# Optimization experiments

Hardware: AMD Instinct MI355X
Metric: run time of the kernel (lower is better)

Reference implementation:

```python
import jax, jax.numpy as jnp
import numpy as np

H = 8      # n_heads
HD = 64    # per-head channels (out_channels in __init__, before *= n_heads)


def setup_inputs() -> dict:
    key = jax.random.key(0)
    ks = jax.random.split(key, 10)
    B, C, N = 4, 256, 2048
    O = H * HD
    s = 1.0 / np.sqrt(C).astype(np.float32)
    return {
        "x": jax.random.normal(ks[0], (B, C, N), dtype=jnp.float32),
        "y": jax.random.normal(ks[1], (B, C, N), dtype=jnp.float32),
        "Wq": jax.random.normal(ks[2], (O, C), dtype=jnp.float32) * s,
        "bq": jnp.zeros((O,), dtype=jnp.float32),
        "Wk": jax.random.normal(ks[3], (O, C), dtype=jnp.float32) * s,
        "bk": jnp.zeros((O,), dtype=jnp.float32),
        "Wv": jax.random.normal(ks[4], (O, C), dtype=jnp.float32) * s,
        "bv": jnp.zeros((O,), dtype=jnp.float32),
        "Wp": jax.random.normal(ks[5], (HD, C), dtype=jnp.float32) * s,  # residual projection, bias=False
        "gamma": jax.random.uniform(ks[6], (H, 1, 1, 1), dtype=jnp.float32) + 0.001,
    }


def _conv1x1(W, b, t):
    # 1x1 Conv1d: (O,C) x (B,C,N) -> (B,O,N)
    out = jnp.einsum('oc,bcn->bon', W, t)
    return out if b is None else out + b[None, :, None]


def _heads(t):
    # (B, H*HD, N) -> (H, B, N, HD); channel split into contiguous per-head chunks
    B, _, N = t.shape
    return t.reshape(B, H, HD, N).transpose(1, 0, 3, 2)


def reference(x, y, Wq, bq, Wk, bk, Wv, bv, Wp, gamma):
    # q/k/v projections via 1x1 convs (kernel_size=1, 'stride_effective' padding => same length)
    q = _heads(_conv1x1(Wq, bq, x))   # (H,B,N,HD)
    k = _heads(_conv1x1(Wk, bk, y))   # (H,B,N,HD)
    v = _heads(_conv1x1(Wv, bv, y))   # (H,B,N,HD)

    # energy = bmm(Q, K^T); softmax over last dim (no mask)
    energy = jnp.einsum('hbnd,hbmd->hbnm', q, k)          # (H,B,N,N)
    attn = jax.nn.softmax(energy, axis=-1)

    # out = bmm(attention.transpose(-2,-1), V)  (note the transpose in the original)
    out = jnp.einsum('hbnm,hbnd->hbmd', attn, v)          # (H,B,N,HD)

    # gamma-weighted residual blend with projected y
    yp = _conv1x1(Wp, None, y).transpose(0, 2, 1)         # (B,N,HD)
    g = gamma.reshape(H, 1, 1, 1)
    out = (g * out + yp[None]) / (1.0 + g)                # (H,B,N,HD)
    return out
```

## Files before the change

kernel.cpp:

```cpp
#include <hip/hip_runtime.h>
#include <math.h>
#include <stdint.h>

#define B_DIM 4
#define C_DIM 256
#define N_DIM 2048
#define H_DIM 8
#define HD    64
#define HB    32
#define NTOK  (B_DIM * N_DIM)
#define LOG2E 1.44269504f

typedef __attribute__((ext_vector_type(8))) short bf16x8;
typedef __attribute__((ext_vector_type(4))) float f32x4;

static __device__ __forceinline__ short f2bf(float f) {
    unsigned u = __builtin_bit_cast(unsigned, f);
    u += 0x7fffu + ((u >> 16) & 1u);
    return (short)(u >> 16);
}
static __device__ __forceinline__ float bf2f(short s) {
    unsigned u = ((unsigned)(unsigned short)s) << 16;
    return __builtin_bit_cast(float, u);
}
static __device__ __forceinline__ float fx2(float x) {
#if __has_builtin(__builtin_amdgcn_exp2f)
    return __builtin_amdgcn_exp2f(x);
#else
    return exp2f(x);
#endif
}
static __device__ __forceinline__ unsigned pk_bf16(float a, float b) {
#if __has_builtin(__builtin_amdgcn_cvt_pk_bf16_f32)
    auto v = __builtin_amdgcn_cvt_pk_bf16_f32(a, b);
    return __builtin_bit_cast(unsigned, v);
#else
    unsigned ua = __builtin_bit_cast(unsigned, a);
    unsigned ub = __builtin_bit_cast(unsigned, b);
    return ((ua + 0x8000u) >> 16) | ((ub + 0x8000u) & 0xffff0000u);
#endif
}

static __device__ __forceinline__ void gll16(const void* g, void* ldsbase, int lane) {
#if __has_builtin(__builtin_amdgcn_global_load_lds)
    __builtin_amdgcn_global_load_lds(
        (const __attribute__((address_space(1))) void*)(uintptr_t)(g),
        (__attribute__((address_space(3))) void*)(uintptr_t)(ldsbase), 16, 0, 0);
#else
    *(bf16x8*)((char*)ldsbase + lane * 16) = *(const bf16x8*)g;
#endif
}

#define MFMA16(A, Bv, Cv) __builtin_amdgcn_mfma_f32_16x16x32_bf16(A, Bv, Cv, 0, 0, 0)


__global__ __launch_bounds__(256) void cast_all(
    const float* __restrict__ X, const float* __restrict__ Y,
    const float* __restrict__ Wq, const float* __restrict__ Wk,
    const float* __restrict__ Wv, const float* __restrict__ Wp,
    short* __restrict__ XS, short* __restrict__ YS,
    short* __restrict__ WSx, short* __restrict__ WSy)
{
    const int z = blockIdx.z;
    const int t = threadIdx.x;

    if (z == 8) {
        int base = (blockIdx.y * 32 + blockIdx.x) * 256 + t;
#pragma unroll
        for (int rep = 0; rep < 2; ++rep) {
            int gid = base + rep * 32768;
            if (gid >= 51200) break;
            int lane = gid & 63, chunk = gid >> 6;
            int lo = lane & 15, quad = lane >> 4;
            const float* src; short* dst;
            if (chunk < 256) {
                int ot = chunk >> 3, ks = chunk & 7;
                src = Wq + (size_t)(ot * 16 + lo) * C_DIM + ks * 32 + quad * 8;
                dst = WSx + (size_t)chunk * 512 + lane * 8;
            } else {
                int ch = chunk - 256;
                int ot = ch >> 3, ks = ch & 7;
                int row = ot * 16 + lo;
                const float* basep = (row < 512) ? (Wk + (size_t)row * C_DIM)
                                   : (row < 1024) ? (Wv + (size_t)(row - 512) * C_DIM)
                                                  : (Wp + (size_t)(row - 1024) * C_DIM);
                src = basep + ks * 32 + quad * 8;
                dst = WSy + (size_t)ch * 512 + lane * 8;
            }
            bf16x8 o;
#pragma unroll
            for (int j = 0; j < 8; ++j) o[j] = f2bf(src[j]);
            *(bf16x8*)dst = o;
        }
        return;
    }

    const float* src = (z < 4) ? X : Y;
    short* dst = (z < 4) ? XS : YS;
    const int b = z & 3, c0 = blockIdx.y * 64, n0 = blockIdx.x * 64;
    __shared__ float L[64][65];
    for (int i = t; i < 4096; i += 256) {
        int cc = i >> 6, nn = i & 63;
        L[cc][nn] = src[((size_t)b * C_DIM + c0 + cc) * N_DIM + n0 + nn];
    }
    __syncthreads();
#pragma unroll
    for (int half = 0; half < 2; ++half) {
        int cid = half * 256 + t;
        int lane = cid & 63, fi = cid >> 6;
        int ksl = fi & 1, rtl = fi >> 1;
        int lo = lane & 15, quad = lane >> 4;
        bf16x8 o;
#pragma unroll
        for (int j = 0; j < 8; ++j) o[j] = f2bf(L[ksl * 32 + quad * 8 + j][rtl * 16 + lo]);
        int rt = b * 128 + (n0 >> 4) + rtl;
        int ks = (c0 >> 5) + ksl;
        *(bf16x8*)(dst + ((size_t)(rt * 8 + ks) * 64 + lane) * 8) = o;
    }
}

__global__ __launch_bounds__(256) void proj_all(
    const short* __restrict__ WSx, const short* __restrict__ WSy,
    const short* __restrict__ XS, const short* __restrict__ YS,
    const float* __restrict__ bq, const float* __restrict__ bk,
    const float* __restrict__ bv,
    short* __restrict__ QS, short* __restrict__ KS,
    short* __restrict__ VSu, float* __restrict__ Yo)
{
    const int oy = blockIdx.y;
    const bool isq = oy < 8;
    const short* WS = isq ? WSx : WSy;
    const short* Xs = isq ? XS : YS;
    const int oyl = isq ? oy : oy - 8;
    const int o0 = oyl * 64;
    const int tok0 = blockIdx.x * 128;
    const int t = threadIdx.x, wave = t >> 6, lane = t & 63;
    const int lo = lane & 15, quad = lane >> 4;

    __shared__ __align__(16) char smem[34816];

    const int ot = oyl * 4 + wave;
    const int rt0 = tok0 >> 4;
    const f32x4 czero = {0.f, 0.f, 0.f, 0.f};

    f32x4 acc[8];
#pragma unroll
    for (int i = 0; i < 8; ++i) acc[i] = czero;

#pragma unroll 2
    for (int ks = 0; ks < 8; ++ks) {
        bf16x8 a = *(const bf16x8*)(WS + ((size_t)(ot * 8 + ks) * 64 + lane) * 8);
#pragma unroll
        for (int nt = 0; nt < 8; ++nt) {
            bf16x8 bx = *(const bf16x8*)(Xs + ((size_t)((rt0 + nt) * 8 + ks) * 64 + lane) * 8);
            acc[nt] = MFMA16(a, bx, acc[nt]);
        }
    }

    const int b = tok0 >> 11;
    const int n0b = tok0 & (N_DIM - 1);

    if (oy < 16) {
        short* T = (short*)smem;
        const float* bias = isq ? bq : bk;
        const float scale = isq ? LOG2E : 1.f;
        float bvr[4];
#pragma unroll
        for (int r = 0; r < 4; ++r) bvr[r] = bias[o0 + wave * 16 + quad * 4 + r];
#pragma unroll
        for (int nt = 0; nt < 8; ++nt) {
            short4 pk;
            pk.x = f2bf((acc[nt][0] + bvr[0]) * scale);
            pk.y = f2bf((acc[nt][1] + bvr[1]) * scale);
            pk.z = f2bf((acc[nt][2] + bvr[2]) * scale);
            pk.w = f2bf((acc[nt][3] + bvr[3]) * scale);
            *(short4*)(T + (nt * 16 + lo) * 72 + wave * 16 + quad * 4) = pk;
        }
        __syncthreads();
        const int h = oyl;
        const int hb = h * 4 + b;
        short* dst = isq ? QS : KS;
#pragma unroll
        for (int s = 0; s < 4; ++s) {
            int cid = s * 256 + t;
            int ln = cid & 63, fi = cid >> 6;
            int ksd = fi & 1, rtl = fi >> 1;
            bf16x8 v = *(const bf16x8*)(T + (rtl * 16 + (ln & 15)) * 72 + ksd * 32 + (ln >> 4) * 8);
            *(bf16x8*)(dst + (((size_t)(hb * 128 + (n0b >> 4) + rtl) * 2 + ksd) * 512 + ln * 8)) = v;
        }
    } else if (oy < 24) {
        short* T2 = (short*)smem;
        float bvr[4];
#pragma unroll
        for (int r = 0; r < 4; ++r) bvr[r] = bv[o0 - 512 + wave * 16 + quad * 4 + r];
#pragma unroll
        for (int nt = 0; nt < 8; ++nt)
#pragma unroll
            for (int r = 0; r < 4; ++r) {
                int ol = wave * 16 + quad * 4 + r;
                T2[ol * 136 + nt * 16 + lo] = f2bf(acc[nt][r] + bvr[r]);
            }
        __syncthreads();
        const int h = oy - 16;
        const int hb = h * 4 + b;
#pragma unroll
        for (int s = 0; s < 4; ++s) {
            int cid = s * 256 + t;
            int ln = cid & 63, fi = cid >> 6;
            int dt = fi & 3, ksd = (fi >> 2) & 1, nbl = fi >> 3;
            int dl = dt * 16 + (ln & 15);
            int tkl = nbl * 64 + ksd * 32 + (ln >> 4) * 8;
            bf16x8 v = *(const bf16x8*)(T2 + dl * 136 + tkl);
            int nbg = (n0b >> 6) + nbl;
            *(bf16x8*)(VSu + ((size_t)(((hb * 32 + nbg) * 2 + ksd) * 4 + dt) * 64 + ln) * 8) = v;
        }
    } else {
        float* T3 = (float*)smem;
#pragma unroll
        for (int nt = 0; nt < 8; ++nt) {
            float4 f;
            f.x = acc[nt][0]; f.y = acc[nt][1]; f.z = acc[nt][2]; f.w = acc[nt][3];
            *(float4*)(T3 + (nt * 16 + lo) * 68 + wave * 16 + quad * 4) = f;
        }
        __syncthreads();
#pragma unroll
        for (int s = 0; s < 8; ++s) {
            int cid = s * 256 + t;
            int row = cid >> 4, c4 = (cid & 15) * 4;
            float4 f = *(const float4*)(T3 + row * 68 + c4);
            *(float4*)(Yo + ((size_t)(tok0 + row)) * 64 + c4) = f;
        }
    }
}

__global__ __launch_bounds__(256, 4) void rowsum_mfma(
    const short* __restrict__ QS, const short* __restrict__ KS,
    float* __restrict__ RSp, float* __restrict__ RSpW)
{
    const int id = blockIdx.x;
    const int hb = ((id & 7) << 2) | ((id >> 3) & 3);
    const int zq = (id >> 5) & 3;
    const int n0 = (id >> 7) * 256;
    const int t = threadIdx.x, wave = t >> 6, lane = t & 63;
    const int lo = lane & 15, quad = lane >> 4;
    const f32x4 czero = {0.f, 0.f, 0.f, 0.f};

    bf16x8 a0[4], a1[4];
#pragma unroll
    for (int s = 0; s < 4; ++s) {
        int rt = (n0 >> 4) + s * 4 + wave;
        a0[s] = *(const bf16x8*)(QS + ((size_t)(hb * 128 + rt) * 2 + 0) * 512 + lane * 8);
        a1[s] = *(const bf16x8*)(QS + ((size_t)(hb * 128 + rt) * 2 + 1) * 512 + lane * 8);
    }

    float sm[4][4];
#pragma unroll
    for (int s = 0; s < 4; ++s)
#pragma unroll
        for (int r = 0; r < 4; ++r) sm[s][r] = 0.f;

    const short* kp = KS + ((size_t)(hb * 128) * 2) * 512 + lane * 8
                    + (size_t)zq * (N_DIM / 4 / 16) * 2 * 512;
    for (int m0 = 0; m0 < N_DIM / 4; m0 += 64) {
#pragma unroll
        for (int mt = 0; mt < 4; ++mt) {
            bf16x8 b0 = *(const bf16x8*)(kp + (mt * 2 + 0) * 512);
            bf16x8 b1 = *(const bf16x8*)(kp + (mt * 2 + 1) * 512);
#pragma unroll
            for (int s = 0; s < 4; ++s) {
                f32x4 c = MFMA16(a0[s], b0, czero);
                c = MFMA16(a1[s], b1, c);
#pragma unroll
                for (int r = 0; r < 4; ++r) sm[s][r] += fx2(c[r]);
            }
        }
        kp += 8 * 512;
    }

#pragma unroll
    for (int sft = 1; sft < 16; sft <<= 1)
#pragma unroll
        for (int s = 0; s < 4; ++s)
#pragma unroll
            for (int r = 0; r < 4; ++r) sm[s][r] += __shfl_xor(sm[s][r], sft);

    if (lo == 0) {
        float* dst = (zq < 2) ? (RSp  + (size_t)zq * HB * N_DIM)
                              : (RSpW + (size_t)(zq - 2) * HB * N_DIM);
#pragma unroll
        for (int s = 0; s < 4; ++s) {
            int row = n0 + s * 64 + wave * 16 + quad * 4;
#pragma unroll
            for (int r = 0; r < 4; ++r)
                dst[(size_t)hb * N_DIM + row + r] = sm[s][r];
        }
    }
}

__global__ __launch_bounds__(256) void v_scale(
    const short* __restrict__ VSu, const float* __restrict__ RSp,
    const float* __restrict__ RSpW, short* __restrict__ VS)
{
    int t = blockIdx.x * 256 + threadIdx.x;
    int lane = t & 63, fidx = t >> 6;
    int ks = (fidx >> 2) & 1, nb = (fidx >> 3) & 31, hb = fidx >> 8;
    int n = nb * 64 + ks * 32 + (lane >> 4) * 8;
    bf16x8 v = *(const bf16x8*)(VSu + (size_t)t * 8);
    const float* r0 = RSp  + (size_t)hb * N_DIM + n;
    const float* r1 = r0 + (size_t)HB * N_DIM;
    const float* r2 = RSpW + (size_t)hb * N_DIM + n;
    const float* r3 = r2 + (size_t)HB * N_DIM;
    bf16x8 o;
#pragma unroll
    for (int j = 0; j < 8; ++j)
        o[j] = f2bf(bf2f(v[j]) / ((r0[j] + r1[j]) + (r2[j] + r3[j])));
    *(bf16x8*)(VS + (size_t)t * 8) = o;
}

__global__ __launch_bounds__(512, 4) void attnout_mfma(
    const short* __restrict__ QS, const short* __restrict__ KS,
    const short* __restrict__ VS,
    short* __restrict__ PA0, short* __restrict__ PA1)
{
    const int id = blockIdx.x;
    const int hb = ((id & 7) << 2) | ((id >> 3) & 3);
    const int z = (id >> 5) & 1;
    const int m0 = (id >> 6) * 128;

    __shared__ __align__(16) char smem[49152];
    short* Pl = (short*)smem;
    char* Qst = smem + 16384;
    char* Vst = smem + 32768;

    const int t = threadIdx.x, wave = t >> 6, lane = t & 63;
    const int lo = lane & 15, quad = lane >> 4;
    const f32x4 czero = {0.f, 0.f, 0.f, 0.f};

    bf16x8 bk0, bk1;
    {
        int rt = (m0 >> 4) + wave;
        bk0 = *(const bf16x8*)(KS + ((size_t)(hb * 128 + rt) * 2 + 0) * 512 + lane * 8);
        bk1 = *(const bf16x8*)(KS + ((size_t)(hb * 128 + rt) * 2 + 1) * 512 + lane * 8);
    }

    f32x4 oacc[4];
#pragma unroll
    for (int dt = 0; dt < 4; ++dt) oacc[dt] = czero;

    const short* qsrc = QS + ((size_t)(hb * 128 + z * 64) * 2) * 512 + lane * 8;
    const short* vsrc = VS + ((size_t)(hb * 32 + z * 16) * 8) * 512 + lane * 8;
    short* prow = Pl + (wave * 16 + lo) * 64;
    const int lh = lo & 7;
    const int NIT = N_DIM / 2 / 64;

    f32x4 c[4];

    gll16(qsrc + (size_t)wave * 512,       Qst + wave * 1024, lane);
    gll16(qsrc + (size_t)(8 + wave) * 512, Qst + 8192 + wave * 1024, lane);
    gll16(vsrc + (size_t)wave * 512,       Vst + wave * 1024, lane);
    __syncthreads();
#pragma unroll
    for (int nt = 0; nt < 4; ++nt) {
        bf16x8 a0 = *(const bf16x8*)(Qst + (nt * 2 + 0) * 1024 + lane * 16);
        bf16x8 a1 = *(const bf16x8*)(Qst + (nt * 2 + 1) * 1024 + lane * 16);
        c[nt] = MFMA16(a0, bk0, czero);
        c[nt] = MFMA16(a1, bk1, c[nt]);
    }
    __syncthreads();

    for (int i = 0; i < NIT - 1; ++i) {
        gll16(qsrc + ((size_t)(i + 2) * 8 + wave) * 512,
              Qst + (i & 1) * 8192 + wave * 1024, lane);
        gll16(vsrc + ((size_t)(i + 1) * 8 + wave) * 512,
              Vst + ((i + 1) & 1) * 8192 + wave * 1024, lane);
#pragma unroll
        for (int nt = 0; nt < 4; ++nt) {
            uint2 pk;
            pk.x = pk_bf16(fx2(c[nt][0]), fx2(c[nt][1]));
            pk.y = pk_bf16(fx2(c[nt][2]), fx2(c[nt][3]));
            int chunk = nt * 2 + (quad >> 1);
            *(uint2*)(prow + (((chunk ^ lh) << 3) | ((quad & 1) << 2))) = pk;
        }
        {
            const char* Qb = Qst + ((i + 1) & 1) * 8192;
            __builtin_amdgcn_s_setprio(1);
#pragma unroll
            for (int nt = 0; nt < 4; ++nt) {
                bf16x8 a0 = *(const bf16x8*)(Qb + (nt * 2 + 0) * 1024 + lane * 16);
                bf16x8 a1 = *(const bf16x8*)(Qb + (nt * 2 + 1) * 1024 + lane * 16);
                c[nt] = MFMA16(a0, bk0, czero);
                c[nt] = MFMA16(a1, bk1, c[nt]);
            }
            __builtin_amdgcn_s_setprio(0);
        }
        {
            const char* vb = Vst + (i & 1) * 8192;
#pragma unroll
            for (int ks = 0; ks < 2; ++ks) {
                bf16x8 ap = *(const bf16x8*)(prow + (((ks * 4 + quad) ^ lh) << 3));
#pragma unroll
                for (int dt = 0; dt < 4; ++dt) {
                    bf16x8 bv = *(const bf16x8*)(vb + (ks * 4 + dt) * 1024 + lane * 16);
                    oacc[dt] = MFMA16(ap, bv, oacc[dt]);
                }
            }
        }
        __syncthreads();
    }

#pragma unroll
    for (int nt = 0; nt < 4; ++nt) {
        uint2 pk;
        pk.x = pk_bf16(fx2(c[nt][0]), fx2(c[nt][1]));
        pk.y = pk_bf16(fx2(c[nt][2]), fx2(c[nt][3]));
        int chunk = nt * 2 + (quad >> 1);
        *(uint2*)(prow + (((chunk ^ lh) << 3) | ((quad & 1) << 2))) = pk;
    }
    {
        const char* vb = Vst + ((NIT - 1) & 1) * 8192;
#pragma unroll
        for (int ks = 0; ks < 2; ++ks) {
            bf16x8 ap = *(const bf16x8*)(prow + (((ks * 4 + quad) ^ lh) << 3));
#pragma unroll
            for (int dt = 0; dt < 4; ++dt) {
                bf16x8 bv = *(const bf16x8*)(vb + (ks * 4 + dt) * 1024 + lane * 16);
                oacc[dt] = MFMA16(ap, bv, oacc[dt]);
            }
        }
    }

    short* PA = z ? PA1 : PA0;
    float* T = (float*)smem;
    __syncthreads();
#pragma unroll
    for (int dt = 0; dt < 4; ++dt)
#pragma unroll
        for (int r = 0; r < 4; ++r)
            T[(wave * 16 + quad * 4 + r) * 68 + dt * 16 + lo] = oacc[dt][r];
    __syncthreads();
#pragma unroll
    for (int it = 0; it < 2; ++it) {
        int idx = it * 512 + t;
        int rowl = idx >> 3, dg = (idx & 7) * 8;
        float4 f0 = *(const float4*)(T + rowl * 68 + dg);
        float4 f1 = *(const float4*)(T + rowl * 68 + dg + 4);
        uint4 o;
        o.x = pk_bf16(f0.x, f0.y);
        o.y = pk_bf16(f0.z, f0.w);
        o.z = pk_bf16(f1.x, f1.y);
        o.w = pk_bf16(f1.z, f1.w);
        int m = m0 + rowl;
        *(uint4*)(PA + ((size_t)(hb * N_DIM + m)) * 64 + dg) = o;
    }
}

__global__ __launch_bounds__(256) void combine_out(
    const short* __restrict__ PA0, const short* __restrict__ PA1,
    const float* __restrict__ YP, const float* __restrict__ gamma,
    float* __restrict__ out)
{
    size_t flat = ((size_t)blockIdx.x * 256 + threadIdx.x) * 8;
    int d  = (int)(flat & 63);
    int n  = (int)((flat >> 6) & (N_DIM - 1));
    int hb = (int)(flat >> 17);
    int h = hb >> 2, b = hb & 3;
    float g = gamma[h];
    float inv = 1.f / (1.f + g);
    float gi = g * inv;
    bf16x8 p0 = *(const bf16x8*)(PA0 + flat);
    bf16x8 p1 = *(const bf16x8*)(PA1 + flat);
    const float* yp = YP + ((size_t)b * N_DIM + n) * HD + d;
    float o[8];
#pragma unroll
    for (int j = 0; j < 8; ++j)
        o[j] = gi * (bf2f(p0[j]) + bf2f(p1[j])) + inv * yp[j];
    float4 o0 = {o[0], o[1], o[2], o[3]};
    float4 o1 = {o[4], o[5], o[6], o[7]};
    *(float4*)(out + flat) = o0;
    *(float4*)(out + flat + 4) = o1;
}

extern "C" void kernel_launch(void* const* d_in, const int* in_sizes, int n_in,
                              void* d_out, int out_size, void* d_ws, size_t ws_size,
                              hipStream_t stream) {
    const float* x     = (const float*)d_in[0];
    const float* y     = (const float*)d_in[1];
    const float* Wq    = (const float*)d_in[2];
    const float* bq    = (const float*)d_in[3];
    const float* Wk    = (const float*)d_in[4];
    const float* bk    = (const float*)d_in[5];
    const float* Wv    = (const float*)d_in[6];
    const float* bv    = (const float*)d_in[7];
    const float* Wp    = (const float*)d_in[8];
    const float* gamma = (const float*)d_in[9];
    float* out = (float*)d_out;

    const size_t XEL  = (size_t)B_DIM * C_DIM * N_DIM;
    const size_t QKV  = (size_t)HB * N_DIM * HD;

    short* XS  = (short*)d_ws;
    short* YS  = XS + XEL;
    short* WSx = YS + XEL;
    short* WSy = WSx + 512 * C_DIM;
    short* QS  = WSy + 1088 * C_DIM;
    short* KS  = QS + QKV;
    short* VSu = KS + QKV;
    short* VS  = VSu + QKV;
    float* YPb = (float*)(VS + QKV);
    float* RSp = YPb + (size_t)B_DIM * N_DIM * HD;
    short* PA0 = XS;
    short* PA1 = VSu;
    float* RSpW = (float*)WSx;

    dim3 blk(256);
    cast_all<<<dim3(N_DIM / 64, C_DIM / 64, 9), blk, 0, stream>>>(
        x, y, Wq, Wk, Wv, Wp, XS, YS, WSx, WSy);

    proj_all<<<dim3(NTOK / 128, 25), blk, 0, stream>>>(
        WSx, WSy, XS, YS, bq, bk, bv, QS, KS, VSu, YPb);

    rowsum_mfma<<<dim3(1024), blk, 0, stream>>>(QS, KS, RSp, RSpW);
    v_scale<<<dim3(2048), blk, 0, stream>>>(VSu, RSp, RSpW, VS);
    attnout_mfma<<<dim3(1024), dim3(512), 0, stream>>>(QS, KS, VS, PA0, PA1);
    combine_out<<<dim3(2048), blk, 0, stream>>>(PA0, PA1, YPb, gamma, out);
}
```

Measured before the change: 188.9 us.

## Switch attention kernels to 32x32x16 MFMA with register-resident P via permlane swap

Moves the rowsum and attention-output kernels from 16x16x32 MFMA tiles to 32x32x16 tiles, and changes the Q/K/V fragment layouts written by the projection kernel to match. In attnout, the exp'd score tile is now converted directly into the A-operand of the PV MFMA in registers using permlane32 swaps, instead of being staged through LDS. That removes the P-tile LDS round trip and lowers the instruction count per FLOP. Blocks shrink from 512 to 256 threads with each wave covering 32 rows, which raises register pressure and may reduce occupancy.

```diff
diff --git a/kernel.cpp b/kernel.cpp
--- a/kernel.cpp
+++ b/kernel.cpp
@@ -13,6 +13,8 @@
 
 typedef __attribute__((ext_vector_type(8))) short bf16x8;
 typedef __attribute__((ext_vector_type(4))) float f32x4;
+typedef __attribute__((ext_vector_type(16))) float f32x16;
+typedef __attribute__((ext_vector_type(4))) unsigned u32x4;
 
 static __device__ __forceinline__ short f2bf(float f) {
     unsigned u = __builtin_bit_cast(unsigned, f);
@@ -40,6 +42,19 @@
     return ((ua + 0x8000u) >> 16) | ((ub + 0x8000u) & 0xffff0000u);
 #endif
 }
+static __device__ __forceinline__ void pl32swap(unsigned &a, unsigned &b) {
+#if __has_builtin(__builtin_amdgcn_permlane32_swap)
+    typedef __attribute__((ext_vector_type(2))) int i32x2_t;
+    i32x2_t r = __builtin_amdgcn_permlane32_swap((int)a, (int)b, false, false);
+    a = (unsigned)r[0]; b = (unsigned)r[1];
+#else
+    unsigned sa = __shfl_xor(a, 32), sb = __shfl_xor(b, 32);
+    bool hi = (threadIdx.x & 32) != 0;
+    unsigned na = hi ? sb : a;
+    unsigned nb = hi ? b : sa;
+    a = na; b = nb;
+#endif
+}
 
 static __device__ __forceinline__ void gll16(const void* g, void* ldsbase, int lane) {
 #if __has_builtin(__builtin_amdgcn_global_load_lds)
@@ -52,6 +67,7 @@
 }
 
 #define MFMA16(A, Bv, Cv) __builtin_amdgcn_mfma_f32_16x16x32_bf16(A, Bv, Cv, 0, 0, 0)
+#define MFMA32(A, Bv, Cv) __builtin_amdgcn_mfma_f32_32x32x16_bf16(A, Bv, Cv, 0, 0, 0)
 
 
 __global__ __launch_bounds__(256) void cast_all(
@@ -184,9 +200,11 @@
         for (int s = 0; s < 4; ++s) {
             int cid = s * 256 + t;
             int ln = cid & 63, fi = cid >> 6;
-            int ksd = fi & 1, rtl = fi >> 1;
-            bf16x8 v = *(const bf16x8*)(T + (rtl * 16 + (ln & 15)) * 72 + ksd * 32 + (ln >> 4) * 8);
-            *(bf16x8*)(dst + (((size_t)(hb * 128 + (n0b >> 4) + rtl) * 2 + ksd) * 512 + ln * 8)) = v;
+            int ks = fi & 3, nt2l = fi >> 2;
+            bf16x8 v = *(const bf16x8*)(T + (nt2l * 32 + (ln & 31)) * 72
+                                          + ks * 16 + ((ln >> 5) << 3));
+            size_t frag = ((size_t)(hb * 64) + (n0b >> 5) + nt2l) * 4 + ks;
+            *(bf16x8*)(dst + frag * 512 + ln * 8) = v;
         }
     } else if (oy < 24) {
         short* T2 = (short*)smem;
@@ -207,12 +225,11 @@
         for (int s = 0; s < 4; ++s) {
             int cid = s * 256 + t;
             int ln = cid & 63, fi = cid >> 6;
-            int dt = fi & 3, ksd = (fi >> 2) & 1, nbl = fi >> 3;
-            int dl = dt * 16 + (ln & 15);
-            int tkl = nbl * 64 + ksd * 32 + (ln >> 4) * 8;
-            bf16x8 v = *(const bf16x8*)(T2 + dl * 136 + tkl);
-            int nbg = (n0b >> 6) + nbl;
-            *(bf16x8*)(VSu + ((size_t)(((hb * 32 + nbg) * 2 + ksd) * 4 + dt) * 64 + ln) * 8) = v;
+            int dt2 = fi & 1, nk = (fi >> 1) & 3, nbl = fi >> 3;
+            bf16x8 v = *(const bf16x8*)(T2 + (dt2 * 32 + (ln & 31)) * 136
+                                           + nbl * 64 + nk * 16 + ((ln >> 5) << 3));
+            size_t frag = (((size_t)(hb * 32) + (n0b >> 6) + nbl) * 4 + nk) * 2 + dt2;
+            *(bf16x8*)(VSu + frag * 512 + ln * 8) = v;
         }
     } else {
         float* T3 = (float*)smem;
@@ -242,58 +259,60 @@
     const int zq = (id >> 5) & 3;
     const int n0 = (id >> 7) * 256;
     const int t = threadIdx.x, wave = t >> 6, lane = t & 63;
-    const int lo = lane & 15, quad = lane >> 4;
-    const f32x4 czero = {0.f, 0.f, 0.f, 0.f};
-
-    bf16x8 a0[4], a1[4];
-#pragma unroll
-    for (int s = 0; s < 4; ++s) {
-        int rt = (n0 >> 4) + s * 4 + wave;
-        a0[s] = *(const bf16x8*)(QS + ((size_t)(hb * 128 + rt) * 2 + 0) * 512 + lane * 8);
-        a1[s] = *(const bf16x8*)(QS + ((size_t)(hb * 128 + rt) * 2 + 1) * 512 + lane * 8);
-    }
-
-    float sm[4][4];
-#pragma unroll
-    for (int s = 0; s < 4; ++s)
-#pragma unroll
-        for (int r = 0; r < 4; ++r) sm[s][r] = 0.f;
-
-    const short* kp = KS + ((size_t)(hb * 128) * 2) * 512 + lane * 8
-                    + (size_t)zq * (N_DIM / 4 / 16) * 2 * 512;
-    for (int m0 = 0; m0 < N_DIM / 4; m0 += 64) {
-#pragma unroll
-        for (int mt = 0; mt < 4; ++mt) {
-            bf16x8 b0 = *(const bf16x8*)(kp + (mt * 2 + 0) * 512);
-            bf16x8 b1 = *(const bf16x8*)(kp + (mt * 2 + 1) * 512);
-#pragma unroll
-            for (int s = 0; s < 4; ++s) {
-                f32x4 c = MFMA16(a0[s], b0, czero);
-                c = MFMA16(a1[s], b1, c);
-#pragma unroll
-                for (int r = 0; r < 4; ++r) sm[s][r] += fx2(c[r]);
-            }
-        }
-        kp += 8 * 512;
-    }
-
-#pragma unroll
-    for (int sft = 1; sft < 16; sft <<= 1)
-#pragma unroll
-        for (int s = 0; s < 4; ++s)
-#pragma unroll
-            for (int r = 0; r < 4; ++r) sm[s][r] += __shfl_xor(sm[s][r], sft);
-
-    if (lo == 0) {
+    const int hi = lane >> 5;
+    f32x16 czero16;
+#pragma unroll
+    for (int r = 0; r < 16; ++r) czero16[r] = 0.f;
+
+    bf16x8 qf[2][4];
+    const short* qb = QS + ((size_t)(hb * 64 + (n0 >> 5) + wave * 2)) * 4 * 512 + lane * 8;
+#pragma unroll
+    for (int tt = 0; tt < 2; ++tt)
+#pragma unroll
+        for (int ks = 0; ks < 4; ++ks)
+            qf[tt][ks] = *(const bf16x8*)(qb + (tt * 4 + ks) * 512);
+
+    float sm[2][16];
+#pragma unroll
+    for (int tt = 0; tt < 2; ++tt)
+#pragma unroll
+        for (int r = 0; r < 16; ++r) sm[tt][r] = 0.f;
+
+    const short* kp = KS + ((size_t)(hb * 64 + zq * 16)) * 4 * 512 + lane * 8;
+    for (int mt = 0; mt < 16; ++mt) {
+        bf16x8 kf[4];
+#pragma unroll
+        for (int ks = 0; ks < 4; ++ks)
+            kf[ks] = *(const bf16x8*)(kp + (mt * 4 + ks) * 512);
+#pragma unroll
+        for (int tt = 0; tt < 2; ++tt) {
+            f32x16 cc = czero16;
+#pragma unroll
+            for (int ks = 0; ks < 4; ++ks) cc = MFMA32(qf[tt][ks], kf[ks], cc);
+#pragma unroll
+            for (int r = 0; r < 16; ++r) sm[tt][r] += fx2(cc[r]);
+        }
+    }
+
+#pragma unroll
+    for (int sft = 1; sft < 32; sft <<= 1)
+#pragma unroll
+        for (int tt = 0; tt < 2; ++tt)
+#pragma unroll
+            for (int r = 0; r < 16; ++r) sm[tt][r] += __shfl_xor(sm[tt][r], sft);
+
+    if ((lane & 31) == 0) {
         float* dst = (zq < 2) ? (RSp  + (size_t)zq * HB * N_DIM)
                               : (RSpW + (size_t)(zq - 2) * HB * N_DIM);
 #pragma unroll
-        for (int s = 0; s < 4; ++s) {
-            int row = n0 + s * 64 + wave * 16 + quad * 4;
-#pragma unroll
-            for (int r = 0; r < 4; ++r)
-                dst[(size_t)hb * N_DIM + row + r] = sm[s][r];
-        }
+        for (int tt = 0; tt < 2; ++tt)
+#pragma unroll
+            for (int g = 0; g < 4; ++g) {
+                int n = n0 + wave * 64 + tt * 32 + g * 8 + hi * 4;
+                float4 v = {sm[tt][g * 4 + 0], sm[tt][g * 4 + 1],
+                            sm[tt][g * 4 + 2], sm[tt][g * 4 + 3]};
+                *(float4*)(dst + (size_t)hb * N_DIM + n) = v;
+            }
     }
 }
 
@@ -303,8 +322,9 @@
 {
     int t = blockIdx.x * 256 + threadIdx.x;
     int lane = t & 63, fidx = t >> 6;
-    int ks = (fidx >> 2) & 1, nb = (fidx >> 3) & 31, hb = fidx >> 8;
-    int n = nb * 64 + ks * 32 + (lane >> 4) * 8;
+    int dt2 = fidx & 1; (void)dt2;
+    int nk = (fidx >> 1) & 3, nb = (fidx >> 3) & 31, hb = fidx >> 8;
+    int n = nb * 64 + nk * 16 + ((lane >> 5) << 3);
     bf16x8 v = *(const bf16x8*)(VSu + (size_t)t * 8);
     const float* r0 = RSp  + (size_t)hb * N_DIM + n;
     const float* r1 = r0 + (size_t)HB * N_DIM;
@@ -317,7 +337,7 @@
     *(bf16x8*)(VS + (size_t)t * 8) = o;
 }
 
-__global__ __launch_bounds__(512, 4) void attnout_mfma(
+__global__ __launch_bounds__(256, 3) void attnout_mfma(
     const short* __restrict__ QS, const short* __restrict__ KS,
     const short* __restrict__ VS,
     short* __restrict__ PA0, short* __restrict__ PA1)
@@ -327,120 +347,145 @@
     const int z = (id >> 5) & 1;
     const int m0 = (id >> 6) * 128;
 
-    __shared__ __align__(16) char smem[49152];
-    short* Pl = (short*)smem;
-    char* Qst = smem + 16384;
-    char* Vst = smem + 32768;
+    __shared__ __align__(16) char smem[34816];
+    char* Qst = smem;
+    char* Vst = smem + 16384;
 
     const int t = threadIdx.x, wave = t >> 6, lane = t & 63;
-    const int lo = lane & 15, quad = lane >> 4;
-    const f32x4 czero = {0.f, 0.f, 0.f, 0.f};
-
-    bf16x8 bk0, bk1;
+    const f32x4 cz4 = {0.f, 0.f, 0.f, 0.f}; (void)cz4;
+    f32x16 czero16;
+#pragma unroll
+    for (int r = 0; r < 16; ++r) czero16[r] = 0.f;
+
+    bf16x8 kf[4];
     {
-        int rt = (m0 >> 4) + wave;
-        bk0 = *(const bf16x8*)(KS + ((size_t)(hb * 128 + rt) * 2 + 0) * 512 + lane * 8);
-        bk1 = *(const bf16x8*)(KS + ((size_t)(hb * 128 + rt) * 2 + 1) * 512 + lane * 8);
-    }
-
-    f32x4 oacc[4];
-#pragma unroll
-    for (int dt = 0; dt < 4; ++dt) oacc[dt] = czero;
-
-    const short* qsrc = QS + ((size_t)(hb * 128 + z * 64) * 2) * 512 + lane * 8;
-    const short* vsrc = VS + ((size_t)(hb * 32 + z * 16) * 8) * 512 + lane * 8;
-    short* prow = Pl + (wave * 16 + lo) * 64;
-    const int lh = lo & 7;
+        const short* kbase = KS + ((size_t)(hb * 64 + (m0 >> 5) + wave)) * 4 * 512 + lane * 8;
+#pragma unroll
+        for (int ks = 0; ks < 4; ++ks)
+            kf[ks] = *(const bf16x8*)(kbase + ks * 512);
+    }
+
+    f32x16 oacc[2];
+#pragma unroll
+    for (int dt2 = 0; dt2 < 2; ++dt2) oacc[dt2] = czero16;
+
+    const short* qsrc = QS + ((size_t)(hb * 64 + z * 32)) * 4 * 512 + lane * 8;
+    const short* vsrc = VS + ((size_t)(hb * 32 + z * 16)) * 8 * 512 + lane * 8;
     const int NIT = N_DIM / 2 / 64;
 
-    f32x4 c[4];
-
-    gll16(qsrc + (size_t)wave * 512,       Qst + wave * 1024, lane);
-    gll16(qsrc + (size_t)(8 + wave) * 512, Qst + 8192 + wave * 1024, lane);
-    gll16(vsrc + (size_t)wave * 512,       Vst + wave * 1024, lane);
+    f32x16 c[2];
+    bf16x8 pa[4];
+
+    gll16(qsrc + (size_t)wave * 512,            Qst + wave * 1024, lane);
+    gll16(qsrc + (size_t)(wave + 4) * 512,      Qst + (wave + 4) * 1024, lane);
+    gll16(qsrc + (size_t)(8 + wave) * 512,      Qst + 8192 + wave * 1024, lane);
+    gll16(qsrc + (size_t)(8 + wave + 4) * 512,  Qst + 8192 + (wave + 4) * 1024, lane);
+    gll16(vsrc + (size_t)wave * 512,            Vst + wave * 1024, lane);
+    gll16(vsrc + (size_t)(wave + 4) * 512,      Vst + (wave + 4) * 1024, lane);
     __syncthreads();
 #pragma unroll
-    for (int nt = 0; nt < 4; ++nt) {
-        bf16x8 a0 = *(const bf16x8*)(Qst + (nt * 2 + 0) * 1024 + lane * 16);
-        bf16x8 a1 = *(const bf16x8*)(Qst + (nt * 2 + 1) * 1024 + lane * 16);
-        c[nt] = MFMA16(a0, bk0, czero);
-        c[nt] = MFMA16(a1, bk1, c[nt]);
+    for (int tt = 0; tt < 2; ++tt) {
+        f32x16 cc = czero16;
+#pragma unroll
+        for (int ks = 0; ks < 4; ++ks) {
+            bf16x8 a = *(const bf16x8*)(Qst + (tt * 4 + ks) * 1024 + lane * 16);
+            cc = MFMA32(a, kf[ks], cc);
+        }
+        c[tt] = cc;
     }
     __syncthreads();
 
     for (int i = 0; i < NIT - 1; ++i) {
         gll16(qsrc + ((size_t)(i + 2) * 8 + wave) * 512,
               Qst + (i & 1) * 8192 + wave * 1024, lane);
+        gll16(qsrc + ((size_t)(i + 2) * 8 + wave + 4) * 512,
+              Qst + (i & 1) * 8192 + (wave + 4) * 1024, lane);
         gll16(vsrc + ((size_t)(i + 1) * 8 + wave) * 512,
               Vst + ((i + 1) & 1) * 8192 + wave * 1024, lane);
-#pragma unroll
-        for (int nt = 0; nt < 4; ++nt) {
-            uint2 pk;
-            pk.x = pk_bf16(fx2(c[nt][0]), fx2(c[nt][1]));
-            pk.y = pk_bf16(fx2(c[nt][2]), fx2(c[nt][3]));
-            int chunk = nt * 2 + (quad >> 1);
-            *(uint2*)(prow + (((chunk ^ lh) << 3) | ((quad & 1) << 2))) = pk;
+        gll16(vsrc + ((size_t)(i + 1) * 8 + wave + 4) * 512,
+              Vst + ((i + 1) & 1) * 8192 + (wave + 4) * 1024, lane);
+#pragma unroll
+        for (int tt = 0; tt < 2; ++tt) {
+#pragma unroll
+            for (int half = 0; half < 2; ++half) {
+                unsigned w01 = pk_bf16(fx2(c[tt][half * 8 + 0]), fx2(c[tt][half * 8 + 1]));
+                unsigned w23 = pk_bf16(fx2(c[tt][half * 8 + 2]), fx2(c[tt][half * 8 + 3]));
+                unsigned w45 = pk_bf16(fx2(c[tt][half * 8 + 4]), fx2(c[tt][half * 8 + 5]));
+                unsigned w67 = pk_bf16(fx2(c[tt][half * 8 + 6]), fx2(c[tt][half * 8 + 7]));
+                pl32swap(w01, w45);
+                pl32swap(w23, w67);
+                u32x4 f = {w01, w23, w45, w67};
+                pa[tt * 2 + half] = __builtin_bit_cast(bf16x8, f);
+            }
         }
         {
             const char* Qb = Qst + ((i + 1) & 1) * 8192;
             __builtin_amdgcn_s_setprio(1);
 #pragma unroll
-            for (int nt = 0; nt < 4; ++nt) {
-                bf16x8 a0 = *(const bf16x8*)(Qb + (nt * 2 + 0) * 1024 + lane * 16);
-                bf16x8 a1 = *(const bf16x8*)(Qb + (nt * 2 + 1) * 1024 + lane * 16);
-                c[nt] = MFMA16(a0, bk0, czero);
-                c[nt] = MFMA16(a1, bk1, c[nt]);
+            for (int tt = 0; tt < 2; ++tt) {
+                f32x16 cc = czero16;
+#pragma unroll
+                for (int ks = 0; ks < 4; ++ks) {
+                    bf16x8 a = *(const bf16x8*)(Qb + (tt * 4 + ks) * 1024 + lane * 16);
+                    cc = MFMA32(a, kf[ks], cc);
+                }
+                c[tt] = cc;
             }
             __builtin_amdgcn_s_setprio(0);
         }
         {
             const char* vb = Vst + (i & 1) * 8192;
 #pragma unroll
-            for (int ks = 0; ks < 2; ++ks) {
-                bf16x8 ap = *(const bf16x8*)(prow + (((ks * 4 + quad) ^ lh) << 3));
-#pragma unroll
-                for (int dt = 0; dt < 4; ++dt) {
-                    bf16x8 bv = *(const bf16x8*)(vb + (ks * 4 + dt) * 1024 + lane * 16);
-                    oacc[dt] = MFMA16(ap, bv, oacc[dt]);
+            for (int nk = 0; nk < 4; ++nk)
+#pragma unroll
+                for (int dt2 = 0; dt2 < 2; ++dt2) {
+                    bf16x8 bv = *(const bf16x8*)(vb + (nk * 2 + dt2) * 1024 + lane * 16);
+                    oacc[dt2] = MFMA32(pa[nk], bv, oacc[dt2]);
                 }
-            }
         }
         __syncthreads();
     }
 
 #pragma unroll
-    for (int nt = 0; nt < 4; ++nt) {
-        uint2 pk;
-        pk.x = pk_bf16(fx2(c[nt][0]), fx2(c[nt][1]));
-        pk.y = pk_bf16(fx2(c[nt][2]), fx2(c[nt][3]));
-        int chunk = nt * 2 + (quad >> 1);
-        *(uint2*)(prow + (((chunk ^ lh) << 3) | ((quad & 1) << 2))) = pk;
+    for (int tt = 0; tt < 2; ++tt) {
+#pragma unroll
+        for (int half = 0; half < 2; ++half) {
+            unsigned w01 = pk_bf16(fx2(c[tt][half * 8 + 0]), fx2(c[tt][half * 8 + 1]));
+            unsigned w23 = pk_bf16(fx2(c[tt][half * 8 + 2]), fx2(c[tt][half * 8 + 3]));
+            unsigned w45 = pk_bf16(fx2(c[tt][half * 8 + 4]), fx2(c[tt][half * 8 + 5]));
+            unsigned w67 = pk_bf16(fx2(c[tt][half * 8 + 6]), fx2(c[tt][half * 8 + 7]));
+            pl32swap(w01, w45);
+            pl32swap(w23, w67);
+            u32x4 f = {w01, w23, w45, w67};
+            pa[tt * 2 + half] = __builtin_bit_cast(bf16x8, f);
+        }
     }
     {
         const char* vb = Vst + ((NIT - 1) & 1) * 8192;
 #pragma unroll
-        for (int ks = 0; ks < 2; ++ks) {
-            bf16x8 ap = *(const bf16x8*)(prow + (((ks * 4 + quad) ^ lh) << 3));
-#pragma unroll
-            for (int dt = 0; dt < 4; ++dt) {
-                bf16x8 bv = *(const bf16x8*)(vb + (ks * 4 + dt) * 1024 + lane * 16);
-                oacc[dt] = MFMA16(ap, bv, oacc[dt]);
+        for (int nk = 0; nk < 4; ++nk)
+#pragma unroll
+            for (int dt2 = 0; dt2 < 2; ++dt2) {
+                bf16x8 bv = *(const bf16x8*)(vb + (nk * 2 + dt2) * 1024 + lane * 16);
+                oacc[dt2] = MFMA32(pa[nk], bv, oacc[dt2]);
             }
-        }
     }
 
     short* PA = z ? PA1 : PA0;
     float* T = (float*)smem;
+    const int hi = lane >> 5;
     __syncthreads();
 #pragma unroll
-    for (int dt = 0; dt < 4; ++dt)
-#pragma unroll
-        for (int r = 0; r < 4; ++r)
-            T[(wave * 16 + quad * 4 + r) * 68 + dt * 16 + lo] = oacc[dt][r];
+    for (int dt2 = 0; dt2 < 2; ++dt2)
+#pragma unroll
+        for (int r = 0; r < 16; ++r) {
+            int row = wave * 32 + (r & 3) + 8 * (r >> 2) + 4 * hi;
+            T[row * 68 + dt2 * 32 + (lane & 31)] = oacc[dt2][r];
+        }
     __syncthreads();
 #pragma unroll
-    for (int it = 0; it < 2; ++it) {
-        int idx = it * 512 + t;
+    for (int it = 0; it < 4; ++it) {
+        int idx = it * 256 + t;
         int rowl = idx >> 3, dg = (idx & 7) * 8;
         float4 f0 = *(const float4*)(T + rowl * 68 + dg);
         float4 f1 = *(const float4*)(T + rowl * 68 + dg + 4);
@@ -521,6 +566,6 @@
 
     rowsum_mfma<<<dim3(1024), blk, 0, stream>>>(QS, KS, RSp, RSpW);
     v_scale<<<dim3(2048), blk, 0, stream>>>(VSu, RSp, RSpW, VS);
-    attnout_mfma<<<dim3(1024), dim3(512), 0, stream>>>(QS, KS, VS, PA0, PA1);
+    attnout_mfma<<<dim3(1024), blk, 0, stream>>>(QS, KS, VS, PA0, PA1);
     combine_out<<<dim3(2048), blk, 0, stream>>>(PA0, PA1, YPb, gamma, out);
 }
```

After: 191.9 us. No clear change (+1.6%).
